# Optimization experiments

Hardware: AMD Instinct MI355X
Metric: run time of the kernel (lower is better)

The kernel has to match this reference:

```python
import jax, jax.numpy as jnp
import numpy as np

HIDDEN = 256    # hidden_channels
NG = 50         # num_gaussians
NF = 128        # num_filters
CUTOFF = 10.0
N_CONF = 100000   # conformer nodes (10 conformers x 10k atoms)
N_GRAPH = 10000   # 2D graph nodes
E_CONF = 1000000  # radius-graph edges
E_GRAPH = 30000   # bond edges
BOND_VOCAB = 5    # bond-feature vocab (BondEncoder)


def setup_inputs() -> dict:
    key = jax.random.key(0)
    ks = jax.random.split(key, 16)
    w = lambda i, shape, scale=0.05: jax.random.normal(ks[i], shape, jnp.float32) * scale
    return dict(
        x=jax.random.normal(ks[0], (N_CONF, HIDDEN), jnp.float32),
        # every graph node owns exactly N_CONF // N_GRAPH conformer nodes (sorted, no empty segments)
        conf_node_batch=jnp.repeat(jnp.arange(N_GRAPH), N_CONF // N_GRAPH),
        edge_index_conf=jax.random.randint(ks[1], (2, E_CONF), 0, N_CONF),
        edge_weight_conf=jax.random.uniform(ks[2], (E_CONF,), jnp.float32) * CUTOFF,
        edge_attr_conf=jax.random.uniform(ks[3], (E_CONF, NG), jnp.float32),
        edge_index_graph=jax.random.randint(ks[4], (2, E_GRAPH), 0, N_GRAPH),
        edge_attr_graph=jax.random.randint(ks[5], (E_GRAPH, 3), 0, BOND_VOCAB),
        # CFConv filter MLP + linear layers
        mlp_w1=w(6, (NG, NF)), mlp_b1=jnp.zeros((NF,), jnp.float32),
        mlp_w2=w(7, (NF, NF)), mlp_b2=jnp.zeros((NF,), jnp.float32),
        cf_lin1=w(8, (HIDDEN, NF)),                      # no bias (SchNet CFConv lin1)
        cf_lin2=w(9, (NF, HIDDEN)), cf_lin2_b=jnp.zeros((HIDDEN,), jnp.float32),
        lin_w=w(10, (HIDDEN, HIDDEN)), lin_b=jnp.zeros((HIDDEN,), jnp.float32),
        # GINConv: bond encoder embeddings (3 features), eps, MLP (Linear-BN-ReLU-Linear)
        bond_emb=w(11, (3, BOND_VOCAB, HIDDEN), 0.1),
        gin_eps=jnp.zeros((), jnp.float32),
        gin_w1=w(12, (HIDDEN, HIDDEN)), gin_b1=jnp.zeros((HIDDEN,), jnp.float32),
        bn1_g=jnp.ones((HIDDEN,), jnp.float32), bn1_b=jnp.zeros((HIDDEN,), jnp.float32),
        gin_w2=w(13, (HIDDEN, HIDDEN)), gin_b2=jnp.zeros((HIDDEN,), jnp.float32),
        # outer BatchNorm1d
        bn2_g=jnp.ones((HIDDEN,), jnp.float32), bn2_b=jnp.zeros((HIDDEN,), jnp.float32),
    )


def _bn(x, g, b, eps=1e-5):
    # training-mode BatchNorm1d (biased variance over the node/batch dim)
    mu = jnp.mean(x, axis=0)
    var = jnp.var(x, axis=0)
    return (x - mu) * jax.lax.rsqrt(var + eps) * g + b


def reference(x, conf_node_batch, edge_index_conf, edge_weight_conf, edge_attr_conf,
              edge_index_graph, edge_attr_graph, mlp_w1, mlp_b1, mlp_w2, mlp_b2,
              cf_lin1, cf_lin2, cf_lin2_b, lin_w, lin_b, bond_emb, gin_eps,
              gin_w1, gin_b1, bn1_g, bn1_b, gin_w2, gin_b2, bn2_g, bn2_b):
    # ---- CFConv branch (use_conf) ----
    C = 0.5 * (jnp.cos(edge_weight_conf * jnp.pi / CUTOFF) + 1.0)          # [E_conf]
    W = jax.nn.relu(edge_attr_conf @ mlp_w1 + mlp_b1) @ mlp_w2 + mlp_b2    # [E_conf, NF]
    W = W * C[:, None]
    xf = x @ cf_lin1                                                       # [N_conf, NF]
    src, dst = edge_index_conf[0], edge_index_conf[1]
    agg = jax.ops.segment_sum(xf[src] * W, dst, num_segments=N_CONF)       # scatter-add
    h = agg @ cf_lin2 + cf_lin2_b                                          # CFConv lin2
    h = jax.nn.relu(h) @ lin_w + lin_b                                     # F.relu then self.lin

    # ---- GIN branch (use_graph) ----
    x_agg = jax.ops.segment_max(x, conf_node_batch, num_segments=N_GRAPH)  # scatter max pool
    e = edge_attr_graph
    edge_emb = bond_emb[0][e[:, 0]] + bond_emb[1][e[:, 1]] + bond_emb[2][e[:, 2]]
    sg, dg = edge_index_graph[0], edge_index_graph[1]
    agg_g = jax.ops.segment_sum(jax.nn.relu(x_agg[sg] + edge_emb), dg, num_segments=N_GRAPH)
    t = (1.0 + gin_eps) * x_agg + agg_g
    t = jax.nn.relu(_bn(t @ gin_w1 + gin_b1, bn1_g, bn1_b)) @ gin_w2 + gin_b2
    x_agg = _bn(t, bn2_g, bn2_b)                                           # outer BN

    # residual=True: out = x + cf_branch + gin_branch[conf_node_batch]
    return x + h + x_agg[conf_node_batch]
```

## Files before the change

### kernel.cpp

```cpp
#include <hip/hip_runtime.h>
#include <hip/hip_bf16.h>
#include <math.h>

#define HIDDEN 256
#define NG 50
#define NF 128
#define NCONF 100000
#define NGRAPH 10000
#define ECONF 1000000
#define EGRAPH 30000
#define PI_OVER_CUTOFF 0.3141592653589793f
#define NBLK 391

typedef __attribute__((ext_vector_type(8))) short bf16x8;
typedef __attribute__((ext_vector_type(4))) float f32x4;

#define AGG_OFF    0ULL
#define XF_OFF     51200000ULL
#define WBUF_OFF   102400000ULL
#define HMID_OFF   102400000ULL
#define XAGG_OFF   358400000ULL
#define AGGG_OFF   368640000ULL
#define TBUF_OFF   378880000ULL
#define UBUF_OFF   389120000ULL
#define STATS_OFF  399360000ULL
#define DEG_OFF    399368192ULL
#define START_OFF  399768192ULL
#define CURS_OFF   400168192ULL
#define BSUM_OFF   400568192ULL
#define SSRC_OFF   400570240ULL
#define SEID_OFF   404570240ULL
#define WS_NEEDED  408570240ULL

#define S_AGG_OFF   0ULL
#define S_XF_OFF    51200000ULL
#define S_HMID_OFF  51200000ULL
#define S_XAGG_OFF  153600000ULL
#define S_AGGG_OFF  163840000ULL
#define S_TBUF_OFF  174080000ULL
#define S_UBUF_OFF  184320000ULL
#define S_STATS_OFF 194560000ULL

template<int EPI>
__global__ __launch_bounds__(256) void gemm128(
    const float* __restrict__ A, const float* __restrict__ B,
    float* __restrict__ C, int M, int N, int K,
    const float* __restrict__ bias,
    const float* __restrict__ xres, const float* __restrict__ gin,
    const int* __restrict__ batch)
{
    __shared__ float As[16][132];
    __shared__ float Bs[16][132];
    const int bm = blockIdx.x * 128;
    const int bn = blockIdx.y * 128;
    const int tid = threadIdx.x;
    const int ty = tid >> 4;
    const int tx = tid & 15;
    float acc[8][8];
#pragma unroll
    for (int i = 0; i < 8; ++i)
#pragma unroll
        for (int j = 0; j < 8; ++j) acc[i][j] = 0.f;

    for (int k0 = 0; k0 < K; k0 += 16) {
#pragma unroll
        for (int i = 0; i < 2; ++i) {
            int f = tid + i * 256;
            int row = f >> 2;
            int c4 = (f & 3) << 2;
            int gr = bm + row;
            float4 v = make_float4(0.f, 0.f, 0.f, 0.f);
            if (gr < M) v = *(const float4*)(A + (size_t)gr * K + k0 + c4);
            As[c4 + 0][row] = v.x;
            As[c4 + 1][row] = v.y;
            As[c4 + 2][row] = v.z;
            As[c4 + 3][row] = v.w;
        }
#pragma unroll
        for (int i = 0; i < 2; ++i) {
            int f = tid + i * 256;
            int row = f >> 5;
            int c4 = (f & 31) << 2;
            *(float4*)&Bs[row][c4] = *(const float4*)(B + (size_t)(k0 + row) * N + bn + c4);
        }
        __syncthreads();
#pragma unroll
        for (int k = 0; k < 16; ++k) {
            float a[8], b[8];
            *(float4*)&a[0] = *(const float4*)&As[k][ty * 8];
            *(float4*)&a[4] = *(const float4*)&As[k][ty * 8 + 4];
            *(float4*)&b[0] = *(const float4*)&Bs[k][tx * 8];
            *(float4*)&b[4] = *(const float4*)&Bs[k][tx * 8 + 4];
#pragma unroll
            for (int i = 0; i < 8; ++i)
#pragma unroll
                for (int j = 0; j < 8; ++j)
                    acc[i][j] = fmaf(a[i], b[j], acc[i][j]);
        }
        __syncthreads();
    }

#pragma unroll
    for (int i = 0; i < 8; ++i) {
        int gr = bm + ty * 8 + i;
        if (gr >= M) continue;
        int gb = 0;
        if (EPI == 2) gb = batch[gr];
#pragma unroll
        for (int jj = 0; jj < 2; ++jj) {
            int c0 = bn + tx * 8 + jj * 4;
            float o[4];
#pragma unroll
            for (int q = 0; q < 4; ++q) o[q] = acc[i][jj * 4 + q];
            if (bias != nullptr) {
                float4 bv = *(const float4*)(bias + c0);
                o[0] += bv.x; o[1] += bv.y; o[2] += bv.z; o[3] += bv.w;
            }
            if (EPI == 1) {
#pragma unroll
                for (int q = 0; q < 4; ++q) o[q] = fmaxf(o[q], 0.f);
            }
            if (EPI == 2) {
                float4 xv = *(const float4*)(xres + (size_t)gr * N + c0);
                float4 gv = *(const float4*)(gin + (size_t)gb * N + c0);
                o[0] += xv.x + gv.x; o[1] += xv.y + gv.y;
                o[2] += xv.z + gv.z; o[3] += xv.w + gv.w;
            }
            *(float4*)(C + (size_t)gr * N + c0) = make_float4(o[0], o[1], o[2], o[3]);
        }
    }
}

__global__ __launch_bounds__(256) void hist_k(const int* __restrict__ ei,
                                              int* __restrict__ deg)
{
    int e = blockIdx.x * 256 + threadIdx.x;
    if (e < ECONF) atomicAdd(&deg[ei[ECONF + e]], 1);
}

__global__ __launch_bounds__(256) void scanA_k(const int* __restrict__ deg,
                                               int* __restrict__ excl,
                                               int* __restrict__ bsum)
{
    __shared__ int s[256];
    int tid = threadIdx.x;
    int i = blockIdx.x * 256 + tid;
    int v = (i < NCONF) ? deg[i] : 0;
    s[tid] = v;
    __syncthreads();
#pragma unroll
    for (int off = 1; off < 256; off <<= 1) {
        int t = (tid >= off) ? s[tid - off] : 0;
        __syncthreads();
        s[tid] += t;
        __syncthreads();
    }
    if (i < NCONF) excl[i] = s[tid] - v;
    if (tid == 255) bsum[blockIdx.x] = s[255];
}

__global__ __launch_bounds__(512) void scanB_k(int* __restrict__ bsum)
{
    __shared__ int s[512];
    int tid = threadIdx.x;
    int v = (tid < NBLK) ? bsum[tid] : 0;
    s[tid] = v;
    __syncthreads();
#pragma unroll
    for (int off = 1; off < 512; off <<= 1) {
        int t = (tid >= off) ? s[tid - off] : 0;
        __syncthreads();
        s[tid] += t;
        __syncthreads();
    }
    if (tid < NBLK) bsum[tid] = s[tid] - v;
}

__global__ __launch_bounds__(256) void scanC_k(int* __restrict__ excl,
                                               const int* __restrict__ bsum)
{
    int i = blockIdx.x * 256 + threadIdx.x;
    if (i < NCONF) excl[i] += bsum[blockIdx.x];
}

__global__ __launch_bounds__(256) void fill_csr_k(const int* __restrict__ ei,
                                                  const int* __restrict__ startx,
                                                  int* __restrict__ cursor,
                                                  int* __restrict__ ssrc,
                                                  int* __restrict__ seid)
{
    int e = blockIdx.x * 256 + threadIdx.x;
    if (e >= ECONF) return;
    int src = ei[e];
    int dst = ei[ECONF + e];
    int pos = atomicAdd(&cursor[dst], 1);
    int slot = startx[dst] + pos;
    ssrc[slot] = src;
    seid[slot] = e;
}

__global__ __launch_bounds__(256) void prep_w_k(const float* __restrict__ w1,
                                                const float* __restrict__ w2,
                                                ushort* __restrict__ w1p,
                                                ushort* __restrict__ w2p)
{
    int t = blockIdx.x * 256 + threadIdx.x;
    if (t < 1024) {
        int l = t & 63;
        int cks = t >> 6;
        int n = (cks >> 1) * 16 + (l & 15);
        int ks = cks & 1;
        ushort out[8];
#pragma unroll
        for (int j = 0; j < 8; ++j) {
            int k = ks * 32 + (l >> 4) * 8 + j;
            float v = (k < NG) ? w1[k * NF + n] : 0.f;
            __hip_bfloat16 h = __float2bfloat16(v);
            out[j] = *(ushort*)&h;
        }
        *(uint4*)(w1p + t * 8) = *(uint4*)out;
    } else if (t < 1024 + 2048) {
        int u = t - 1024;
        int l = u & 63;
        int cks = u >> 6;
        int n = (cks >> 2) * 16 + (l & 15);
        int ks = cks & 3;
        ushort out[8];
#pragma unroll
        for (int j = 0; j < 8; ++j) {
            int k = ks * 32 + (l >> 4) * 8 + j;
            float v = w2[k * NF + n];
            __hip_bfloat16 h = __float2bfloat16(v);
            out[j] = *(ushort*)&h;
        }
        *(uint4*)(w2p + u * 8) = *(uint4*)out;
    }
}

__global__ __launch_bounds__(256) void edge_mlp_mfma_k(
    const float* __restrict__ EA, const ushort* __restrict__ w1p,
    const float* __restrict__ b1, const ushort* __restrict__ w2p,
    const float* __restrict__ b2, const float* __restrict__ ew,
    ushort* __restrict__ Wout)
{
    __shared__ ushort ea_lds[64 * 64];
    __shared__ ushort t_lds[64 * 128];
    __shared__ float ccs[64];

    const int tid = threadIdx.x;
    const int e0 = blockIdx.x * 64;

    {
        int row = tid >> 2, q = tid & 3;
        const float* rp = EA + (size_t)(e0 + row) * NG;
        char* base = (char*)ea_lds + row * 128;
        int swz = (row & 7) << 4;
#pragma unroll
        for (int p = 0; p < 8; ++p) {
            int k = q * 16 + p * 2;
            float2 v = make_float2(0.f, 0.f);
            if (k < NG) v = *(const float2*)(rp + k);
            __hip_bfloat16 h0 = __float2bfloat16(v.x);
            __hip_bfloat16 h1 = __float2bfloat16(v.y);
            uint pk = (uint)(*(ushort*)&h0) | ((uint)(*(ushort*)&h1) << 16);
            *(uint*)(base + ((k * 2) ^ swz)) = pk;
        }
    }
    if (tid < 64)
        ccs[tid] = 0.5f * (cosf(ew[e0 + tid] * PI_OVER_CUTOFF) + 1.0f);
    __syncthreads();

    const int wv = tid >> 6;
    const int l = tid & 63;
    const int l15 = l & 15, lhi = l >> 4;
    const int arow = wv * 16 + l15;
    const int aswz = (arow & 7) << 4;

    bf16x8 a1[2];
    {
        const char* eab = (const char*)ea_lds + arow * 128;
        a1[0] = *(const bf16x8*)(eab + ((0 + lhi * 16) ^ aswz));
        a1[1] = *(const bf16x8*)(eab + ((64 + lhi * 16) ^ aswz));
    }
    f32x4 acc1[8];
#pragma unroll
    for (int ct = 0; ct < 8; ++ct) {
        float bb = b1[ct * 16 + l15];
        acc1[ct][0] = bb; acc1[ct][1] = bb; acc1[ct][2] = bb; acc1[ct][3] = bb;
    }
#pragma unroll
    for (int ct = 0; ct < 8; ++ct) {
#pragma unroll
        for (int ks = 0; ks < 2; ++ks) {
            bf16x8 bfr = *(const bf16x8*)(w1p + ((size_t)(ct * 2 + ks) * 64 + l) * 8);
            acc1[ct] = __builtin_amdgcn_mfma_f32_16x16x32_bf16(a1[ks], bfr, acc1[ct], 0, 0, 0);
        }
    }
#pragma unroll
    for (int ct = 0; ct < 8; ++ct) {
#pragma unroll
        for (int q = 0; q < 4; ++q) {
            int row = wv * 16 + lhi * 4 + q;
            int col = ct * 16 + l15;
            float v = fmaxf(acc1[ct][q], 0.f);
            __hip_bfloat16 h = __float2bfloat16(v);
            *(ushort*)((char*)t_lds + ((row * 256 + col * 2) ^ ((row & 7) << 4))) = *(ushort*)&h;
        }
    }
    __syncthreads();

    bf16x8 a2[4];
    {
        const char* tb = (const char*)t_lds + arow * 256;
#pragma unroll
        for (int ks = 0; ks < 4; ++ks)
            a2[ks] = *(const bf16x8*)(tb + ((ks * 64 + lhi * 16) ^ aswz));
    }
    f32x4 acc2[8];
#pragma unroll
    for (int ct = 0; ct < 8; ++ct) {
        float bb = b2[ct * 16 + l15];
        acc2[ct][0] = bb; acc2[ct][1] = bb; acc2[ct][2] = bb; acc2[ct][3] = bb;
    }
#pragma unroll
    for (int ct = 0; ct < 8; ++ct) {
#pragma unroll
        for (int ks = 0; ks < 4; ++ks) {
            bf16x8 bfr = *(const bf16x8*)(w2p + ((size_t)(ct * 4 + ks) * 64 + l) * 8);
            acc2[ct] = __builtin_amdgcn_mfma_f32_16x16x32_bf16(a2[ks], bfr, acc2[ct], 0, 0, 0);
        }
    }

    float ccr[4];
#pragma unroll
    for (int q = 0; q < 4; ++q) ccr[q] = ccs[wv * 16 + lhi * 4 + q];
#pragma unroll
    for (int ct = 0; ct < 8; ++ct) {
#pragma unroll
        for (int q = 0; q < 4; ++q) {
            int row = wv * 16 + lhi * 4 + q;
            int col = ct * 16 + l15;
            __hip_bfloat16 h = __float2bfloat16(acc2[ct][q] * ccr[q]);
            Wout[(size_t)(e0 + row) * NF + col] = *(ushort*)&h;
        }
    }
}

__global__ __launch_bounds__(256) void gather_k(
    const int* __restrict__ startx, const int* __restrict__ deg,
    const int* __restrict__ seid, const int* __restrict__ ssrc,
    const __hip_bfloat16* __restrict__ Wbuf, const float* __restrict__ xf,
    float* __restrict__ agg)
{
    int d = blockIdx.x * 2 + (threadIdx.x >> 7);
    int c = threadIdx.x & 127;
    int s0 = startx[d];
    int n = deg[d];
    float acc = 0.f;
    for (int i = 0; i < n; ++i) {
        int e = seid[s0 + i];
        int src = ssrc[s0 + i];
        float w = __bfloat162float(Wbuf[(size_t)e * NF + c]);
        acc = fmaf(w, xf[(size_t)src * NF + c], acc);
    }
    agg[(size_t)d * NF + c] = acc;
}

__global__ __launch_bounds__(256) void edge_mlp_scatter(
    const float* __restrict__ EA, const float* __restrict__ w1,
    const float* __restrict__ b1, const float* __restrict__ w2,
    const float* __restrict__ b2, const float* __restrict__ ew,
    const int* __restrict__ ei, const float* __restrict__ xf,
    float* __restrict__ agg)
{
    __shared__ float w1s[NG * NF];
    __shared__ float b1s[NF];
    __shared__ float w2s[NF * NF];
    __shared__ float b2s[NF];
    __shared__ float eas[64 * NG];
    __shared__ float ts[64 * 132];

    const int tid = threadIdx.x;
    for (int i = tid; i < NG * NF / 4; i += 256)
        ((float4*)w1s)[i] = ((const float4*)w1)[i];
    for (int i = tid; i < NF * NF / 4; i += 256)
        ((float4*)w2s)[i] = ((const float4*)w2)[i];
    if (tid < NF / 4) ((float4*)b1s)[tid] = ((const float4*)b1)[tid];
    else if (tid < NF / 2) ((float4*)b2s)[tid - NF / 4] = ((const float4*)b2)[tid - NF / 4];

    const int e0 = blockIdx.x * 64;
    for (int i = tid; i < 64 * NG / 4; i += 256)
        ((float4*)eas)[i] = ((const float4*)(EA + (size_t)e0 * NG))[i];
    __syncthreads();

    const int tr = tid >> 4;
    const int tc = tid & 15;

    float acc[4][8];
#pragma unroll
    for (int i = 0; i < 4; ++i)
#pragma unroll
        for (int j = 0; j < 8; ++j) acc[i][j] = b1s[tc * 8 + j];
    for (int k = 0; k < NG; ++k) {
        float b[8];
        *(float4*)&b[0] = *(const float4*)&w1s[k * NF + tc * 8];
        *(float4*)&b[4] = *(const float4*)&w1s[k * NF + tc * 8 + 4];
#pragma unroll
        for (int i = 0; i < 4; ++i) {
            float a = eas[(tr * 4 + i) * NG + k];
#pragma unroll
            for (int j = 0; j < 8; ++j) acc[i][j] = fmaf(a, b[j], acc[i][j]);
        }
    }
#pragma unroll
    for (int i = 0; i < 4; ++i)
#pragma unroll
        for (int jj = 0; jj < 2; ++jj) {
            float4 v;
            v.x = fmaxf(acc[i][jj * 4 + 0], 0.f);
            v.y = fmaxf(acc[i][jj * 4 + 1], 0.f);
            v.z = fmaxf(acc[i][jj * 4 + 2], 0.f);
            v.w = fmaxf(acc[i][jj * 4 + 3], 0.f);
            *(float4*)&ts[(tr * 4 + i) * 132 + tc * 8 + jj * 4] = v;
        }
    __syncthreads();

    float acc2[4][8];
#pragma unroll
    for (int i = 0; i < 4; ++i)
#pragma unroll
        for (int j = 0; j < 8; ++j) acc2[i][j] = b2s[tc * 8 + j];
    for (int k = 0; k < NF; ++k) {
        float b[8];
        *(float4*)&b[0] = *(const float4*)&w2s[k * NF + tc * 8];
        *(float4*)&b[4] = *(const float4*)&w2s[k * NF + tc * 8 + 4];
#pragma unroll
        for (int i = 0; i < 4; ++i) {
            float a = ts[(tr * 4 + i) * 132 + k];
#pragma unroll
            for (int j = 0; j < 8; ++j) acc2[i][j] = fmaf(a, b[j], acc2[i][j]);
        }
    }

#pragma unroll
    for (int i = 0; i < 4; ++i) {
        int e = e0 + tr * 4 + i;
        int src = ei[e];
        int dst = ei[ECONF + e];
        float cc = 0.5f * (cosf(ew[e] * PI_OVER_CUTOFF) + 1.0f);
        float4 x0 = *(const float4*)(xf + (size_t)src * NF + tc * 8);
        float4 x1 = *(const float4*)(xf + (size_t)src * NF + tc * 8 + 4);
        float xv[8] = { x0.x, x0.y, x0.z, x0.w, x1.x, x1.y, x1.z, x1.w };
        float* ap = agg + (size_t)dst * NF + tc * 8;
#pragma unroll
        for (int j = 0; j < 8; ++j)
            atomicAdd(ap + j, cc * acc2[i][j] * xv[j]);
    }
}

__global__ __launch_bounds__(256) void seg_max_k(const float* __restrict__ x,
                                                 float* __restrict__ xagg)
{
    int g = blockIdx.x;
    int c = threadIdx.x;
    float m = -INFINITY;
#pragma unroll
    for (int r = 0; r < NCONF / NGRAPH; ++r)
        m = fmaxf(m, x[((size_t)g * (NCONF / NGRAPH) + r) * HIDDEN + c]);
    xagg[(size_t)g * HIDDEN + c] = m;
}

__global__ __launch_bounds__(256) void gin_edge_k(const float* __restrict__ xagg,
                                                  const float* __restrict__ bemb,
                                                  const int* __restrict__ eig,
                                                  const int* __restrict__ eag,
                                                  float* __restrict__ aggg)
{
    int e = blockIdx.x;
    int c = threadIdx.x;
    int sg = eig[e];
    int dg = eig[EGRAPH + e];
    int f0 = eag[e * 3 + 0];
    int f1 = eag[e * 3 + 1];
    int f2 = eag[e * 3 + 2];
    float v = xagg[(size_t)sg * HIDDEN + c]
            + bemb[(0 * 5 + f0) * HIDDEN + c]
            + bemb[(1 * 5 + f1) * HIDDEN + c]
            + bemb[(2 * 5 + f2) * HIDDEN + c];
    v = fmaxf(v, 0.f);
    atomicAdd(&aggg[(size_t)dg * HIDDEN + c], v);
}

__global__ __launch_bounds__(256) void gin_t_k(const float* __restrict__ xagg,
                                               const float* __restrict__ aggg,
                                               const float* __restrict__ epsp,
                                               float* __restrict__ t)
{
    int idx = blockIdx.x * 256 + threadIdx.x;
    float e1 = 1.f + epsp[0];
    float4 a = ((const float4*)xagg)[idx];
    float4 g = ((const float4*)aggg)[idx];
    ((float4*)t)[idx] = make_float4(e1 * a.x + g.x, e1 * a.y + g.y,
                                    e1 * a.z + g.z, e1 * a.w + g.w);
}

__global__ __launch_bounds__(256) void bn_stats_k(const float* __restrict__ u, int M,
                                                  float* __restrict__ sums)
{
    int c = threadIdx.x;
    int r0 = blockIdx.x * 256;
    int rend = min(r0 + 256, M);
    float s = 0.f, s2 = 0.f;
    for (int r = r0; r < rend; ++r) {
        float v = u[(size_t)r * HIDDEN + c];
        s += v;
        s2 = fmaf(v, v, s2);
    }
    atomicAdd(&sums[c], s);
    atomicAdd(&sums[HIDDEN + c], s2);
}

__global__ __launch_bounds__(256) void bn_final_k(const float* __restrict__ sums,
                                                  const float* __restrict__ g,
                                                  const float* __restrict__ b,
                                                  int M, float* __restrict__ ss)
{
    int c = threadIdx.x;
    float mean = sums[c] / (float)M;
    float var = sums[HIDDEN + c] / (float)M - mean * mean;
    float sc = g[c] / sqrtf(var + 1e-5f);
    ss[c] = sc;
    ss[HIDDEN + c] = b[c] - mean * sc;
}

template<bool RELU>
__global__ __launch_bounds__(256) void bn_apply_k(const float* __restrict__ u,
                                                  const float* __restrict__ ss,
                                                  float* __restrict__ out)
{
    int idx = blockIdx.x * 256 + threadIdx.x;
    int c4 = (idx & (HIDDEN / 4 - 1)) * 4;
    float4 v = ((const float4*)u)[idx];
    float4 sc = *(const float4*)&ss[c4];
    float4 sh = *(const float4*)&ss[HIDDEN + c4];
    float4 o = make_float4(v.x * sc.x + sh.x, v.y * sc.y + sh.y,
                           v.z * sc.z + sh.z, v.w * sc.w + sh.w);
    if (RELU) {
        o.x = fmaxf(o.x, 0.f); o.y = fmaxf(o.y, 0.f);
        o.z = fmaxf(o.z, 0.f); o.w = fmaxf(o.w, 0.f);
    }
    ((float4*)out)[idx] = o;
}

extern "C" void kernel_launch(void* const* d_in, const int* in_sizes, int n_in,
                              void* d_out, int out_size, void* d_ws, size_t ws_size,
                              hipStream_t stream)
{
    const float* x        = (const float*)d_in[0];
    const int*   cnb      = (const int*)d_in[1];
    const int*   eic      = (const int*)d_in[2];
    const float* ewc      = (const float*)d_in[3];
    const float* eac      = (const float*)d_in[4];
    const int*   eig      = (const int*)d_in[5];
    const int*   eag      = (const int*)d_in[6];
    const float* mlp_w1   = (const float*)d_in[7];
    const float* mlp_b1   = (const float*)d_in[8];
    const float* mlp_w2   = (const float*)d_in[9];
    const float* mlp_b2   = (const float*)d_in[10];
    const float* cf_lin1  = (const float*)d_in[11];
    const float* cf_lin2  = (const float*)d_in[12];
    const float* cf_lin2b = (const float*)d_in[13];
    const float* lin_w    = (const float*)d_in[14];
    const float* lin_b    = (const float*)d_in[15];
    const float* bond_emb = (const float*)d_in[16];
    const float* gin_eps  = (const float*)d_in[17];
    const float* gin_w1   = (const float*)d_in[18];
    const float* gin_b1   = (const float*)d_in[19];
    const float* bn1_g    = (const float*)d_in[20];
    const float* bn1_b    = (const float*)d_in[21];
    const float* gin_w2   = (const float*)d_in[22];
    const float* gin_b2   = (const float*)d_in[23];
    const float* bn2_g    = (const float*)d_in[24];
    const float* bn2_b    = (const float*)d_in[25];
    float* out = (float*)d_out;

    char* ws = (char*)d_ws;
    const bool big = (ws_size >= WS_NEEDED);

    float* agg, *xf, *hmid, *xagg, *aggg, *tbuf, *ubuf, *sums1, *ss1, *sums2, *ss2;
    if (big) {
        agg  = (float*)(ws + AGG_OFF);
        xf   = (float*)(ws + XF_OFF);
        hmid = (float*)(ws + HMID_OFF);
        xagg = (float*)(ws + XAGG_OFF);
        aggg = (float*)(ws + AGGG_OFF);
        tbuf = (float*)(ws + TBUF_OFF);
        ubuf = (float*)(ws + UBUF_OFF);
        sums1 = (float*)(ws + STATS_OFF);
    } else {
        agg  = (float*)(ws + S_AGG_OFF);
        xf   = (float*)(ws + S_XF_OFF);
        hmid = (float*)(ws + S_HMID_OFF);
        xagg = (float*)(ws + S_XAGG_OFF);
        aggg = (float*)(ws + S_AGGG_OFF);
        tbuf = (float*)(ws + S_TBUF_OFF);
        ubuf = (float*)(ws + S_UBUF_OFF);
        sums1 = (float*)(ws + S_STATS_OFF);
    }
    ss1   = sums1 + 512;
    sums2 = sums1 + 1024;
    ss2   = sums1 + 1536;
    float* gout = aggg;

    hipMemsetAsync(aggg, 0, (size_t)NGRAPH * HIDDEN * 4, stream);
    hipMemsetAsync(sums1, 0, 8192, stream);

    seg_max_k<<<NGRAPH, 256, 0, stream>>>(x, xagg);

    gemm128<0><<<dim3(782, 1), 256, 0, stream>>>(x, cf_lin1, xf, NCONF, NF, HIDDEN,
                                                 nullptr, nullptr, nullptr, nullptr);

    if (big) {
        ushort* Wbuf  = (ushort*)(ws + WBUF_OFF);
        int* deg      = (int*)(ws + DEG_OFF);
        int* startx   = (int*)(ws + START_OFF);
        int* cursor   = (int*)(ws + CURS_OFF);
        int* bsum     = (int*)(ws + BSUM_OFF);
        int* ssrc     = (int*)(ws + SSRC_OFF);
        int* seid     = (int*)(ws + SEID_OFF);
        ushort* w1p   = (ushort*)(ws + AGG_OFF);
        ushort* w2p   = (ushort*)(ws + AGG_OFF + 16384);

        hipMemsetAsync(deg, 0, 400000, stream);
        hipMemsetAsync(cursor, 0, 400000, stream);

        prep_w_k<<<12, 256, 0, stream>>>(mlp_w1, mlp_w2, w1p, w2p);

        hist_k<<<(ECONF + 255) / 256, 256, 0, stream>>>(eic, deg);
        scanA_k<<<NBLK, 256, 0, stream>>>(deg, startx, bsum);
        scanB_k<<<1, 512, 0, stream>>>(bsum);
        scanC_k<<<NBLK, 256, 0, stream>>>(startx, bsum);
        fill_csr_k<<<(ECONF + 255) / 256, 256, 0, stream>>>(eic, startx, cursor, ssrc, seid);

        edge_mlp_mfma_k<<<ECONF / 64, 256, 0, stream>>>(eac, w1p, mlp_b1, w2p, mlp_b2,
                                                        ewc, Wbuf);
        gather_k<<<NCONF / 2, 256, 0, stream>>>(startx, deg, seid, ssrc,
                                                (const __hip_bfloat16*)Wbuf, xf, agg);
    } else {
        hipMemsetAsync(agg, 0, (size_t)NCONF * NF * 4, stream);
        edge_mlp_scatter<<<ECONF / 64, 256, 0, stream>>>(eac, mlp_w1, mlp_b1, mlp_w2,
                                                         mlp_b2, ewc, eic, xf, agg);
    }

    gemm128<1><<<dim3(782, 2), 256, 0, stream>>>(agg, cf_lin2, hmid, NCONF, HIDDEN, NF,
                                                 cf_lin2b, nullptr, nullptr, nullptr);

    gin_edge_k<<<EGRAPH, 256, 0, stream>>>(xagg, bond_emb, eig, eag, aggg);
    gin_t_k<<<NGRAPH * HIDDEN / 4 / 256, 256, 0, stream>>>(xagg, aggg, gin_eps, tbuf);
    gemm128<0><<<dim3(79, 2), 256, 0, stream>>>(tbuf, gin_w1, ubuf, NGRAPH, HIDDEN, HIDDEN,
                                                gin_b1, nullptr, nullptr, nullptr);
    bn_stats_k<<<(NGRAPH + 255) / 256, 256, 0, stream>>>(ubuf, NGRAPH, sums1);
    bn_final_k<<<1, 256, 0, stream>>>(sums1, bn1_g, bn1_b, NGRAPH, ss1);
    bn_apply_k<true><<<NGRAPH * HIDDEN / 4 / 256, 256, 0, stream>>>(ubuf, ss1, tbuf);
    gemm128<0><<<dim3(79, 2), 256, 0, stream>>>(tbuf, gin_w2, ubuf, NGRAPH, HIDDEN, HIDDEN,
                                                gin_b2, nullptr, nullptr, nullptr);
    bn_stats_k<<<(NGRAPH + 255) / 256, 256, 0, stream>>>(ubuf, NGRAPH, sums2);
    bn_final_k<<<1, 256, 0, stream>>>(sums2, bn2_g, bn2_b, NGRAPH, ss2);
    bn_apply_k<false><<<NGRAPH * HIDDEN / 4 / 256, 256, 0, stream>>>(ubuf, ss2, gout);

    gemm128<2><<<dim3(782, 2), 256, 0, stream>>>(hmid, lin_w, out, NCONF, HIDDEN, HIDDEN,
                                                 lin_b, x, gout, cnb);
}
```

Measured before the change: 1.597 ms.

## Use bf16 MFMA GEMMs, bf16 intermediates, and CSR-ordered edge filter output

Replaces the fp32 gemm128 node GEMMs (lin1, lin2, lin) with a bf16 MFMA kernel that reads pre-packed bf16 weights. xf, agg and hmid are now stored as bf16. The edge MLP now runs in CSR (sorted) order through seid, so the gather reads Wbuf contiguously per slot, and each thread handles 8 channels with vector loads. This cuts intermediate memory traffic and the random gather of Wbuf rows. The cost is lower precision in several intermediates and a random read of edge attributes inside the edge MLP.

```diff
diff --git a/kernel.cpp b/kernel.cpp
--- a/kernel.cpp
+++ b/kernel.cpp
@@ -15,22 +15,35 @@
 typedef __attribute__((ext_vector_type(8))) short bf16x8;
 typedef __attribute__((ext_vector_type(4))) float f32x4;
 
-#define AGG_OFF    0ULL
-#define XF_OFF     51200000ULL
-#define WBUF_OFF   102400000ULL
-#define HMID_OFF   102400000ULL
-#define XAGG_OFF   358400000ULL
-#define AGGG_OFF   368640000ULL
-#define TBUF_OFF   378880000ULL
-#define UBUF_OFF   389120000ULL
-#define STATS_OFF  399360000ULL
-#define DEG_OFF    399368192ULL
-#define START_OFF  399768192ULL
-#define CURS_OFF   400168192ULL
-#define BSUM_OFF   400568192ULL
-#define SSRC_OFF   400570240ULL
-#define SEID_OFF   404570240ULL
-#define WS_NEEDED  408570240ULL
+__device__ inline ushort f2b(float v) {
+    __hip_bfloat16 h = __float2bfloat16(v);
+    return *(ushort*)&h;
+}
+__device__ inline float b2f(ushort u) {
+    union { uint i; float f; } c; c.i = (uint)u << 16; return c.f;
+}
+
+#define XFB_OFF    0ULL
+#define AGGB_OFF   25600000ULL
+#define WBUF_OFF   51200000ULL
+#define HMIDB_OFF  51200000ULL
+#define XAGG_OFF   307200000ULL
+#define AGGG_OFF   317440000ULL
+#define TBUF_OFF   327680000ULL
+#define UBUF_OFF   337920000ULL
+#define STATS_OFF  348160000ULL
+#define DEG_OFF    348168192ULL
+#define START_OFF  348568192ULL
+#define CURS_OFF   348968192ULL
+#define BSUM_OFF   349368192ULL
+#define SSRC_OFF   349370240ULL
+#define SEID_OFF   353370240ULL
+#define W1P_OFF    357370240ULL
+#define W2P_OFF    357386624ULL
+#define L1P_OFF    357419392ULL
+#define L2P_OFF    357484928ULL
+#define LWP_OFF    357550464ULL
+#define WS_NEEDED  357681536ULL
 
 #define S_AGG_OFF   0ULL
 #define S_XF_OFF    51200000ULL
@@ -131,6 +144,95 @@
     }
 }
 
+template<int EPI, int KD, int ND, typename AT>
+__global__ __launch_bounds__(256) void gemm_mfma(
+    const AT* __restrict__ A, const ushort* __restrict__ Bp,
+    void* __restrict__ Cv, int M,
+    const float* __restrict__ bias,
+    const float* __restrict__ xres, const float* __restrict__ gin,
+    const int* __restrict__ batch)
+{
+    __shared__ ushort a_lds[64 * KD];
+    const int tid = threadIdx.x;
+    const int bm = blockIdx.x * 64;
+
+    {
+        int row = tid >> 2, q = tid & 3;
+        int gr = bm + row;
+        char* base = (char*)a_lds + row * (KD * 2);
+        int swz = (row & 7) << 4;
+        const AT* rp = A + (size_t)gr * KD;
+#pragma unroll
+        for (int p = 0; p < KD / 32; ++p) {
+            int k = q * (KD / 4) + p * 8;
+            uint4 pk = make_uint4(0, 0, 0, 0);
+            if (gr < M) {
+                if constexpr (sizeof(AT) == 4) {
+                    float4 v0 = *(const float4*)(rp + k);
+                    float4 v1 = *(const float4*)(rp + k + 4);
+                    ushort o[8] = { f2b(v0.x), f2b(v0.y), f2b(v0.z), f2b(v0.w),
+                                    f2b(v1.x), f2b(v1.y), f2b(v1.z), f2b(v1.w) };
+                    pk = *(uint4*)o;
+                } else {
+                    pk = *(const uint4*)(rp + k);
+                }
+            }
+            *(uint4*)(base + ((k * 2) ^ swz)) = pk;
+        }
+    }
+    __syncthreads();
+
+    const int wv = tid >> 6, l = tid & 63, l15 = l & 15, lhi = l >> 4;
+    const int arow = wv * 16 + l15, aswz = (arow & 7) << 4;
+
+    bf16x8 a[KD / 32];
+    const char* ab = (const char*)a_lds + arow * (KD * 2);
+#pragma unroll
+    for (int ks = 0; ks < KD / 32; ++ks)
+        a[ks] = *(const bf16x8*)(ab + ((ks * 64 + lhi * 16) ^ aswz));
+
+    f32x4 acc[ND / 16];
+#pragma unroll
+    for (int nt = 0; nt < ND / 16; ++nt) {
+        float bb = 0.f;
+        if constexpr (EPI != 0) bb = bias[nt * 16 + l15];
+        acc[nt][0] = bb; acc[nt][1] = bb; acc[nt][2] = bb; acc[nt][3] = bb;
+    }
+#pragma unroll
+    for (int nt = 0; nt < ND / 16; ++nt)
+#pragma unroll
+        for (int ks = 0; ks < KD / 32; ++ks) {
+            bf16x8 bfr = *(const bf16x8*)(Bp + ((size_t)(nt * (KD / 32) + ks) * 64 + l) * 8);
+            acc[nt] = __builtin_amdgcn_mfma_f32_16x16x32_bf16(a[ks], bfr, acc[nt], 0, 0, 0);
+        }
+
+    int gb[4];
+    if constexpr (EPI == 2) {
+#pragma unroll
+        for (int q = 0; q < 4; ++q) {
+            int gr = bm + wv * 16 + lhi * 4 + q;
+            gb[q] = (gr < M) ? batch[gr] : 0;
+        }
+    }
+#pragma unroll
+    for (int nt = 0; nt < ND / 16; ++nt) {
+        int col = nt * 16 + l15;
+#pragma unroll
+        for (int q = 0; q < 4; ++q) {
+            int gr = bm + wv * 16 + lhi * 4 + q;
+            if (gr >= M) continue;
+            float v = acc[nt][q];
+            if constexpr (EPI == 1) v = fmaxf(v, 0.f);
+            if constexpr (EPI <= 1) {
+                ((ushort*)Cv)[(size_t)gr * ND + col] = f2b(v);
+            } else {
+                v += xres[(size_t)gr * ND + col] + gin[(size_t)gb[q] * ND + col];
+                ((float*)Cv)[(size_t)gr * ND + col] = v;
+            }
+        }
+    }
+}
+
 __global__ __launch_bounds__(256) void hist_k(const int* __restrict__ ei,
                                               int* __restrict__ deg)
 {
@@ -214,9 +316,7 @@
 #pragma unroll
         for (int j = 0; j < 8; ++j) {
             int k = ks * 32 + (l >> 4) * 8 + j;
-            float v = (k < NG) ? w1[k * NF + n] : 0.f;
-            __hip_bfloat16 h = __float2bfloat16(v);
-            out[j] = *(ushort*)&h;
+            out[j] = (k < NG) ? f2b(w1[k * NF + n]) : (ushort)0;
         }
         *(uint4*)(w1p + t * 8) = *(uint4*)out;
     } else if (t < 1024 + 2048) {
@@ -229,18 +329,38 @@
 #pragma unroll
         for (int j = 0; j < 8; ++j) {
             int k = ks * 32 + (l >> 4) * 8 + j;
-            float v = w2[k * NF + n];
-            __hip_bfloat16 h = __float2bfloat16(v);
-            out[j] = *(ushort*)&h;
+            out[j] = f2b(w2[k * NF + n]);
         }
         *(uint4*)(w2p + u * 8) = *(uint4*)out;
     }
+}
+
+__global__ __launch_bounds__(256) void prep_pack_k(const float* __restrict__ w,
+                                                   ushort* __restrict__ wp,
+                                                   int K, int N)
+{
+    int t = blockIdx.x * 256 + threadIdx.x;
+    int total = (N / 16) * (K / 32) * 64;
+    if (t >= total) return;
+    int l = t & 63;
+    int cks = t >> 6;
+    int nks = K / 32;
+    int nt = cks / nks, ks = cks - nt * nks;
+    int n = nt * 16 + (l & 15);
+    ushort out[8];
+#pragma unroll
+    for (int j = 0; j < 8; ++j) {
+        int k = ks * 32 + (l >> 4) * 8 + j;
+        out[j] = f2b(w[k * N + n]);
+    }
+    *(uint4*)(wp + t * 8) = *(uint4*)out;
 }
 
 __global__ __launch_bounds__(256) void edge_mlp_mfma_k(
     const float* __restrict__ EA, const ushort* __restrict__ w1p,
     const float* __restrict__ b1, const ushort* __restrict__ w2p,
     const float* __restrict__ b2, const float* __restrict__ ew,
+    const int* __restrict__ seid,
     ushort* __restrict__ Wout)
 {
     __shared__ ushort ea_lds[64 * 64];
@@ -252,7 +372,8 @@
 
     {
         int row = tid >> 2, q = tid & 3;
-        const float* rp = EA + (size_t)(e0 + row) * NG;
+        int e = seid[e0 + row];
+        const float* rp = EA + (size_t)e * NG;
         char* base = (char*)ea_lds + row * 128;
         int swz = (row & 7) << 4;
 #pragma unroll
@@ -260,14 +381,12 @@
             int k = q * 16 + p * 2;
             float2 v = make_float2(0.f, 0.f);
             if (k < NG) v = *(const float2*)(rp + k);
-            __hip_bfloat16 h0 = __float2bfloat16(v.x);
-            __hip_bfloat16 h1 = __float2bfloat16(v.y);
-            uint pk = (uint)(*(ushort*)&h0) | ((uint)(*(ushort*)&h1) << 16);
+            uint pk = (uint)f2b(v.x) | ((uint)f2b(v.y) << 16);
             *(uint*)(base + ((k * 2) ^ swz)) = pk;
         }
     }
     if (tid < 64)
-        ccs[tid] = 0.5f * (cosf(ew[e0 + tid] * PI_OVER_CUTOFF) + 1.0f);
+        ccs[tid] = 0.5f * (cosf(ew[seid[e0 + tid]] * PI_OVER_CUTOFF) + 1.0f);
     __syncthreads();
 
     const int wv = tid >> 6;
@@ -289,24 +408,21 @@
         acc1[ct][0] = bb; acc1[ct][1] = bb; acc1[ct][2] = bb; acc1[ct][3] = bb;
     }
 #pragma unroll
-    for (int ct = 0; ct < 8; ++ct) {
+    for (int ct = 0; ct < 8; ++ct)
 #pragma unroll
         for (int ks = 0; ks < 2; ++ks) {
             bf16x8 bfr = *(const bf16x8*)(w1p + ((size_t)(ct * 2 + ks) * 64 + l) * 8);
             acc1[ct] = __builtin_amdgcn_mfma_f32_16x16x32_bf16(a1[ks], bfr, acc1[ct], 0, 0, 0);
         }
-    }
-#pragma unroll
-    for (int ct = 0; ct < 8; ++ct) {
+#pragma unroll
+    for (int ct = 0; ct < 8; ++ct)
 #pragma unroll
         for (int q = 0; q < 4; ++q) {
             int row = wv * 16 + lhi * 4 + q;
             int col = ct * 16 + l15;
-            float v = fmaxf(acc1[ct][q], 0.f);
-            __hip_bfloat16 h = __float2bfloat16(v);
-            *(ushort*)((char*)t_lds + ((row * 256 + col * 2) ^ ((row & 7) << 4))) = *(ushort*)&h;
-        }
-    }
+            *(ushort*)((char*)t_lds + ((row * 256 + col * 2) ^ ((row & 7) << 4))) =
+                f2b(fmaxf(acc1[ct][q], 0.f));
+        }
     __syncthreads();
 
     bf16x8 a2[4];
@@ -323,47 +439,52 @@
         acc2[ct][0] = bb; acc2[ct][1] = bb; acc2[ct][2] = bb; acc2[ct][3] = bb;
     }
 #pragma unroll
-    for (int ct = 0; ct < 8; ++ct) {
+    for (int ct = 0; ct < 8; ++ct)
 #pragma unroll
         for (int ks = 0; ks < 4; ++ks) {
             bf16x8 bfr = *(const bf16x8*)(w2p + ((size_t)(ct * 4 + ks) * 64 + l) * 8);
             acc2[ct] = __builtin_amdgcn_mfma_f32_16x16x32_bf16(a2[ks], bfr, acc2[ct], 0, 0, 0);
         }
-    }
 
     float ccr[4];
 #pragma unroll
     for (int q = 0; q < 4; ++q) ccr[q] = ccs[wv * 16 + lhi * 4 + q];
 #pragma unroll
-    for (int ct = 0; ct < 8; ++ct) {
+    for (int ct = 0; ct < 8; ++ct)
 #pragma unroll
         for (int q = 0; q < 4; ++q) {
             int row = wv * 16 + lhi * 4 + q;
             int col = ct * 16 + l15;
-            __hip_bfloat16 h = __float2bfloat16(acc2[ct][q] * ccr[q]);
-            Wout[(size_t)(e0 + row) * NF + col] = *(ushort*)&h;
-        }
-    }
+            Wout[(size_t)(e0 + row) * NF + col] = f2b(acc2[ct][q] * ccr[q]);
+        }
 }
 
 __global__ __launch_bounds__(256) void gather_k(
     const int* __restrict__ startx, const int* __restrict__ deg,
-    const int* __restrict__ seid, const int* __restrict__ ssrc,
-    const __hip_bfloat16* __restrict__ Wbuf, const float* __restrict__ xf,
-    float* __restrict__ agg)
-{
-    int d = blockIdx.x * 2 + (threadIdx.x >> 7);
-    int c = threadIdx.x & 127;
+    const int* __restrict__ ssrc,
+    const ushort* __restrict__ Wbuf, const ushort* __restrict__ xfb,
+    ushort* __restrict__ aggb)
+{
+    int d = blockIdx.x * 16 + (threadIdx.x >> 4);
+    int c0 = (threadIdx.x & 15) * 8;
     int s0 = startx[d];
     int n = deg[d];
-    float acc = 0.f;
+    float acc[8] = {0.f, 0.f, 0.f, 0.f, 0.f, 0.f, 0.f, 0.f};
     for (int i = 0; i < n; ++i) {
-        int e = seid[s0 + i];
-        int src = ssrc[s0 + i];
-        float w = __bfloat162float(Wbuf[(size_t)e * NF + c]);
-        acc = fmaf(w, xf[(size_t)src * NF + c], acc);
-    }
-    agg[(size_t)d * NF + c] = acc;
+        int slot = s0 + i;
+        int src = ssrc[slot];
+        uint4 wv4 = *(const uint4*)(Wbuf + (size_t)slot * NF + c0);
+        uint4 xv4 = *(const uint4*)(xfb + (size_t)src * NF + c0);
+        const ushort* wu = (const ushort*)&wv4;
+        const ushort* xu = (const ushort*)&xv4;
+#pragma unroll
+        for (int j = 0; j < 8; ++j)
+            acc[j] = fmaf(b2f(wu[j]), b2f(xu[j]), acc[j]);
+    }
+    ushort o[8];
+#pragma unroll
+    for (int j = 0; j < 8; ++j) o[j] = f2b(acc[j]);
+    *(uint4*)(aggb + (size_t)d * NF + c0) = *(uint4*)o;
 }
 
 __global__ __launch_bounds__(256) void edge_mlp_scatter(
@@ -587,54 +708,46 @@
     char* ws = (char*)d_ws;
     const bool big = (ws_size >= WS_NEEDED);
 
-    float* agg, *xf, *hmid, *xagg, *aggg, *tbuf, *ubuf, *sums1, *ss1, *sums2, *ss2;
     if (big) {
-        agg  = (float*)(ws + AGG_OFF);
-        xf   = (float*)(ws + XF_OFF);
-        hmid = (float*)(ws + HMID_OFF);
-        xagg = (float*)(ws + XAGG_OFF);
-        aggg = (float*)(ws + AGGG_OFF);
-        tbuf = (float*)(ws + TBUF_OFF);
-        ubuf = (float*)(ws + UBUF_OFF);
-        sums1 = (float*)(ws + STATS_OFF);
-    } else {
-        agg  = (float*)(ws + S_AGG_OFF);
-        xf   = (float*)(ws + S_XF_OFF);
-        hmid = (float*)(ws + S_HMID_OFF);
-        xagg = (float*)(ws + S_XAGG_OFF);
-        aggg = (float*)(ws + S_AGGG_OFF);
-        tbuf = (float*)(ws + S_TBUF_OFF);
-        ubuf = (float*)(ws + S_UBUF_OFF);
-        sums1 = (float*)(ws + S_STATS_OFF);
-    }
-    ss1   = sums1 + 512;
-    sums2 = sums1 + 1024;
-    ss2   = sums1 + 1536;
-    float* gout = aggg;
-
-    hipMemsetAsync(aggg, 0, (size_t)NGRAPH * HIDDEN * 4, stream);
-    hipMemsetAsync(sums1, 0, 8192, stream);
-
-    seg_max_k<<<NGRAPH, 256, 0, stream>>>(x, xagg);
-
-    gemm128<0><<<dim3(782, 1), 256, 0, stream>>>(x, cf_lin1, xf, NCONF, NF, HIDDEN,
-                                                 nullptr, nullptr, nullptr, nullptr);
-
-    if (big) {
+        ushort* xfb   = (ushort*)(ws + XFB_OFF);
+        ushort* aggb  = (ushort*)(ws + AGGB_OFF);
         ushort* Wbuf  = (ushort*)(ws + WBUF_OFF);
+        ushort* hmidb = (ushort*)(ws + HMIDB_OFF);
+        float* xagg   = (float*)(ws + XAGG_OFF);
+        float* aggg   = (float*)(ws + AGGG_OFF);
+        float* tbuf   = (float*)(ws + TBUF_OFF);
+        float* ubuf   = (float*)(ws + UBUF_OFF);
+        float* sums1  = (float*)(ws + STATS_OFF);
+        float* ss1    = sums1 + 512;
+        float* sums2  = sums1 + 1024;
+        float* ss2    = sums1 + 1536;
         int* deg      = (int*)(ws + DEG_OFF);
         int* startx   = (int*)(ws + START_OFF);
         int* cursor   = (int*)(ws + CURS_OFF);
         int* bsum     = (int*)(ws + BSUM_OFF);
         int* ssrc     = (int*)(ws + SSRC_OFF);
         int* seid     = (int*)(ws + SEID_OFF);
-        ushort* w1p   = (ushort*)(ws + AGG_OFF);
-        ushort* w2p   = (ushort*)(ws + AGG_OFF + 16384);
-
+        ushort* w1p   = (ushort*)(ws + W1P_OFF);
+        ushort* w2p   = (ushort*)(ws + W2P_OFF);
+        ushort* l1p   = (ushort*)(ws + L1P_OFF);
+        ushort* l2p   = (ushort*)(ws + L2P_OFF);
+        ushort* lwp   = (ushort*)(ws + LWP_OFF);
+        float* gout   = aggg;
+
+        hipMemsetAsync(aggg, 0, (size_t)NGRAPH * HIDDEN * 4, stream);
+        hipMemsetAsync(sums1, 0, 8192, stream);
         hipMemsetAsync(deg, 0, 400000, stream);
         hipMemsetAsync(cursor, 0, 400000, stream);
 
         prep_w_k<<<12, 256, 0, stream>>>(mlp_w1, mlp_w2, w1p, w2p);
+        prep_pack_k<<<16, 256, 0, stream>>>(cf_lin1, l1p, 256, 128);
+        prep_pack_k<<<16, 256, 0, stream>>>(cf_lin2, l2p, 128, 256);
+        prep_pack_k<<<32, 256, 0, stream>>>(lin_w,   lwp, 256, 256);
+
+        seg_max_k<<<NGRAPH, 256, 0, stream>>>(x, xagg);
+
+        gemm_mfma<0, 256, 128, float><<<1563, 256, 0, stream>>>(
+            x, l1p, xfb, NCONF, nullptr, nullptr, nullptr, nullptr);
 
         hist_k<<<(ECONF + 255) / 256, 256, 0, stream>>>(eic, deg);
         scanA_k<<<NBLK, 256, 0, stream>>>(deg, startx, bsum);
@@ -643,31 +756,65 @@
         fill_csr_k<<<(ECONF + 255) / 256, 256, 0, stream>>>(eic, startx, cursor, ssrc, seid);
 
         edge_mlp_mfma_k<<<ECONF / 64, 256, 0, stream>>>(eac, w1p, mlp_b1, w2p, mlp_b2,
-                                                        ewc, Wbuf);
-        gather_k<<<NCONF / 2, 256, 0, stream>>>(startx, deg, seid, ssrc,
-                                                (const __hip_bfloat16*)Wbuf, xf, agg);
+                                                        ewc, seid, Wbuf);
+        gather_k<<<NCONF / 16, 256, 0, stream>>>(startx, deg, ssrc, Wbuf, xfb, aggb);
+
+        gemm_mfma<1, 128, 256, ushort><<<1563, 256, 0, stream>>>(
+            aggb, l2p, hmidb, NCONF, cf_lin2b, nullptr, nullptr, nullptr);
+
+        gin_edge_k<<<EGRAPH, 256, 0, stream>>>(xagg, bond_emb, eig, eag, aggg);
+        gin_t_k<<<NGRAPH * HIDDEN / 4 / 256, 256, 0, stream>>>(xagg, aggg, gin_eps, tbuf);
+        gemm128<0><<<dim3(79, 2), 256, 0, stream>>>(tbuf, gin_w1, ubuf, NGRAPH, HIDDEN,
+                                                    HIDDEN, gin_b1, nullptr, nullptr, nullptr);
+        bn_stats_k<<<(NGRAPH + 255) / 256, 256, 0, stream>>>(ubuf, NGRAPH, sums1);
+        bn_final_k<<<1, 256, 0, stream>>>(sums1, bn1_g, bn1_b, NGRAPH, ss1);
+        bn_apply_k<true><<<NGRAPH * HIDDEN / 4 / 256, 256, 0, stream>>>(ubuf, ss1, tbuf);
+        gemm128<0><<<dim3(79, 2), 256, 0, stream>>>(tbuf, gin_w2, ubuf, NGRAPH, HIDDEN,
+                                                    HIDDEN, gin_b2, nullptr, nullptr, nullptr);
+        bn_stats_k<<<(NGRAPH + 255) / 256, 256, 0, stream>>>(ubuf, NGRAPH, sums2);
+        bn_final_k<<<1, 256, 0, stream>>>(sums2, bn2_g, bn2_b, NGRAPH, ss2);
+        bn_apply_k<false><<<NGRAPH * HIDDEN / 4 / 256, 256, 0, stream>>>(ubuf, ss2, gout);
+
+        gemm_mfma<2, 256, 256, ushort><<<1563, 256, 0, stream>>>(
+            hmidb, lwp, out, NCONF, lin_b, x, gout, cnb);
     } else {
+        float* agg   = (float*)(ws + S_AGG_OFF);
+        float* xf    = (float*)(ws + S_XF_OFF);
+        float* hmid  = (float*)(ws + S_HMID_OFF);
+        float* xagg  = (float*)(ws + S_XAGG_OFF);
+        float* aggg  = (float*)(ws + S_AGGG_OFF);
+        float* tbuf  = (float*)(ws + S_TBUF_OFF);
+        float* ubuf  = (float*)(ws + S_UBUF_OFF);
+        float* sums1 = (float*)(ws + S_STATS_OFF);
+        float* ss1   = sums1 + 512;
+        float* sums2 = sums1 + 1024;
+        float* ss2   = sums1 + 1536;
+        float* gout  = aggg;
+
         hipMemsetAsync(agg, 0, (size_t)NCONF * NF * 4, stream);
+        hipMemsetAsync(aggg, 0, (size_t)NGRAPH * HIDDEN * 4, stream);
+        hipMemsetAsync(sums1, 0, 8192, stream);
+
+        seg_max_k<<<NGRAPH, 256, 0, stream>>>(x, xagg);
+        gemm128<0><<<dim3(782, 1), 256, 0, stream>>>(x, cf_lin1, xf, NCONF, NF, HIDDEN,
+                                                     nullptr, nullptr, nullptr, nullptr);
         edge_mlp_scatter<<<ECONF / 64, 256, 0, stream>>>(eac, mlp_w1, mlp_b1, mlp_w2,
                                                          mlp_b2, ewc, eic, xf, agg);
-    }
-
-    gemm128<1><<<dim3(782, 2), 256, 0, stream>>>(agg, cf_lin2, hmid, NCONF, HIDDEN, NF,
-                                                 cf_lin2b, nullptr, nullptr, nullptr);
-
-    gin_edge_k<<<EGRAPH, 256, 0, stream>>>(xagg, bond_emb, eig, eag, aggg);
-    gin_t_k<<<NGRAPH * HIDDEN / 4 / 256, 256, 0, stream>>>(xagg, aggg, gin_eps, tbuf);
-    gemm128<0><<<dim3(79, 2), 256, 0, stream>>>(tbuf, gin_w1, ubuf, NGRAPH, HIDDEN, HIDDEN,
-                                                gin_b1, nullptr, nullptr, nullptr);
-    bn_stats_k<<<(NGRAPH + 255) / 256, 256, 0, stream>>>(ubuf, NGRAPH, sums1);
-    bn_final_k<<<1, 256, 0, stream>>>(sums1, bn1_g, bn1_b, NGRAPH, ss1);
-    bn_apply_k<true><<<NGRAPH * HIDDEN / 4 / 256, 256, 0, stream>>>(ubuf, ss1, tbuf);
-    gemm128<0><<<dim3(79, 2), 256, 0, stream>>>(tbuf, gin_w2, ubuf, NGRAPH, HIDDEN, HIDDEN,
-                                                gin_b2, nullptr, nullptr, nullptr);
-    bn_stats_k<<<(NGRAPH + 255) / 256, 256, 0, stream>>>(ubuf, NGRAPH, sums2);
-    bn_final_k<<<1, 256, 0, stream>>>(sums2, bn2_g, bn2_b, NGRAPH, ss2);
-    bn_apply_k<false><<<NGRAPH * HIDDEN / 4 / 256, 256, 0, stream>>>(ubuf, ss2, gout);
-
-    gemm128<2><<<dim3(782, 2), 256, 0, stream>>>(hmid, lin_w, out, NCONF, HIDDEN, HIDDEN,
-                                                 lin_b, x, gout, cnb);
-}
+        gemm128<1><<<dim3(782, 2), 256, 0, stream>>>(agg, cf_lin2, hmid, NCONF, HIDDEN,
+                                                     NF, cf_lin2b, nullptr, nullptr, nullptr);
+        gin_edge_k<<<EGRAPH, 256, 0, stream>>>(xagg, bond_emb, eig, eag, aggg);
+        gin_t_k<<<NGRAPH * HIDDEN / 4 / 256, 256, 0, stream>>>(xagg, aggg, gin_eps, tbuf);
+        gemm128<0><<<dim3(79, 2), 256, 0, stream>>>(tbuf, gin_w1, ubuf, NGRAPH, HIDDEN,
+                                                    HIDDEN, gin_b1, nullptr, nullptr, nullptr);
+        bn_stats_k<<<(NGRAPH + 255) / 256, 256, 0, stream>>>(ubuf, NGRAPH, sums1);
+        bn_final_k<<<1, 256, 0, stream>>>(sums1, bn1_g, bn1_b, NGRAPH, ss1);
+        bn_apply_k<true><<<NGRAPH * HIDDEN / 4 / 256, 256, 0, stream>>>(ubuf, ss1, tbuf);
+        gemm128<0><<<dim3(79, 2), 256, 0, stream>>>(tbuf, gin_w2, ubuf, NGRAPH, HIDDEN,
+                                                    HIDDEN, gin_b2, nullptr, nullptr, nullptr);
+        bn_stats_k<<<(NGRAPH + 255) / 256, 256, 0, stream>>>(ubuf, NGRAPH, sums2);
+        bn_final_k<<<1, 256, 0, stream>>>(sums2, bn2_g, bn2_b, NGRAPH, ss2);
+        bn_apply_k<false><<<NGRAPH * HIDDEN / 4 / 256, 256, 0, stream>>>(ubuf, ss2, gout);
+        gemm128<2><<<dim3(782, 2), 256, 0, stream>>>(hmid, lin_w, out, NCONF, HIDDEN,
+                                                     HIDDEN, lin_b, x, gout, cnb);
+    }
+}
```

After: 1.332 ms. -16.6%, faster.
